# Kernel tuning notes

Measured on AMD Instinct MI355X. Metric: run time of the kernel, lower is better.

## Reference

```python
import jax, jax.numpy as jnp
import numpy as np
from jax import lax

NUM_CLASSES = 21      # VOC: background (class 0) + 20 fg classes
TOP_K = 200           # max detections kept per (image, class)
CONF_THRESH = 0.01
NMS_THRESH = 0.45
VAR0, VAR1 = 0.1, 0.2 # cfg.VARIANCE
K_PRE = 256           # candidates pre-selected per class before NMS (fixed-shape NMS)


def setup_inputs() -> dict:
    key = jax.random.key(0)
    k1, k2, k3 = jax.random.split(key, 3)
    B, P, C = 32, 8732, NUM_CLASSES
    loc_data = jax.random.normal(k1, (B, P, 4), dtype=jnp.float32)
    conf_data = jax.random.normal(k2, (B, P, C), dtype=jnp.float32)
    u = jax.random.uniform(k3, (P, 4), dtype=jnp.float32)
    # priors in center-offset form: centers in [0,1), w/h in [0.02, 0.32)
    prior_data = jnp.concatenate([u[:, :2], 0.02 + 0.3 * u[:, 2:]], axis=-1)
    return {"loc_data": loc_data, "conf_data": conf_data, "prior_data": prior_data}


def decode(loc, priors):
    # loc, priors: [..., 4]; priors are (cx, cy, w, h)
    centers = priors[..., :2] + loc[..., :2] * VAR0 * priors[..., 2:]
    wh = priors[..., 2:] * jnp.exp(loc[..., 2:] * VAR1)
    xy_min = centers - wh * 0.5
    return jnp.concatenate([xy_min, xy_min + wh], axis=-1)  # (x1,y1,x2,y2)


def pairwise_iou(b):
    # b: [K, 4] corner boxes -> [K, K] IoU
    area = jnp.maximum(b[:, 2] - b[:, 0], 0.0) * jnp.maximum(b[:, 3] - b[:, 1], 0.0)
    lt = jnp.maximum(b[:, None, :2], b[None, :, :2])
    rb = jnp.minimum(b[:, None, 2:], b[None, :, 2:])
    wh = jnp.clip(rb - lt, 0.0)
    inter = wh[..., 0] * wh[..., 1]
    union = area[:, None] + area[None, :] - inter
    return inter / jnp.maximum(union, 1e-9)


def nms_one_class(scores_p, boxes_p4):
    # scores_p: [P], boxes_p4: [P, 4]; fixed-shape NMS -> [TOP_K, 5] (score, x1, y1, x2, y2)
    vals, idx = lax.top_k(scores_p, K_PRE)          # sorted descending
    cand = boxes_p4[idx]                            # [K_PRE, 4]
    valid = vals > CONF_THRESH
    iou = pairwise_iou(cand)                        # [K_PRE, K_PRE]
    ar = jnp.arange(K_PRE)

    def step(keep, i):
        # a kept box suppresses later boxes overlapping it above threshold
        sup = keep[i] & (iou[i] > NMS_THRESH) & (ar > i)
        return keep & (~sup), None

    keep, _ = lax.scan(step, valid, ar)
    kept_scores = jnp.where(keep, vals, 0.0)
    # kept entries are already score-ordered; pull the top TOP_K survivors to the front
    sv, si = lax.top_k(kept_scores, TOP_K)
    out_boxes = jnp.where(sv[:, None] > 0.0, cand[si], 0.0)
    return jnp.concatenate([sv[:, None], out_boxes], axis=-1)  # [TOP_K, 5]


def reference(loc_data, conf_data, prior_data):
    # loc_data: [B, P, 4], conf_data: [B, P, C], prior_data: [P, 4]
    probs = jax.nn.softmax(conf_data, axis=-1)                     # [B, P, C]
    probs_fg = jnp.swapaxes(probs[..., 1:], 1, 2)                  # [B, C-1, P] (skip background)
    boxes = decode(loc_data, prior_data[None, :, :])               # [B, P, 4]
    # vmap over classes, then over batch
    per_class = jax.vmap(nms_one_class, in_axes=(0, None))         # ([C-1,P],[P,4]) -> [C-1,TOP_K,5]
    per_image = jax.vmap(per_class, in_axes=(0, 0))
    return per_image(probs_fg, boxes)                              # [B, C-1, TOP_K, 5]
```

## Files before the change

kernel.cpp:

```cpp
#include <hip/hip_runtime.h>
#include <stdint.h>

typedef unsigned long long ull;

#define NUM_CLASSES 21
#define NFG 20
#define TOPK 200
#define KPRE 256
#define CONF_TH 0.01f
#define NMS_TH 0.45f
#define VAR0 0.1f
#define VAR1 0.2f
#define NVMAX 35
#define BITS_CONF 0x3C23D70Au
#define BITS_ONE1 0x3F800001u
#define BSLOT(g) ((g) + ((g) >> 6))

__global__ __launch_bounds__(256) void softmax_probs_kernel(
    const float* __restrict__ conf, float* __restrict__ probs, int P) {
    __shared__ __align__(16) float obuf[NFG * 256];
    const int t = threadIdx.x;
    const int b = blockIdx.y;
    const int p0 = blockIdx.x << 8;
    const int cnt = min(256, P - p0);

    if (t < cnt) {
        const float* row = conf + ((size_t)b * P + p0 + t) * NUM_CLASSES;
        float x[NUM_CLASSES];
        float mx = row[0];
        x[0] = mx;
#pragma unroll
        for (int j = 1; j < NUM_CLASSES; ++j) { x[j] = row[j]; mx = fmaxf(mx, x[j]); }
        float s = 0.f;
#pragma unroll
        for (int j = 0; j < NUM_CLASSES; ++j) { x[j] = expf(x[j] - mx); s += x[j]; }
#pragma unroll
        for (int c = 1; c < NUM_CLASSES; ++c)
            obuf[(c - 1) * 256 + t] = x[c] / s;
    }
    __syncthreads();

    float* dst = probs + ((size_t)b * NFG) * P + p0;
    if (cnt == 256) {
#pragma unroll
        for (int k = 0; k < 5; ++k) {
            int e = (k << 8) + t;
            int c = e >> 6;
            int f = e & 63;
            float4 val = ((const float4*)obuf)[(c << 6) + f];
            *(float4*)(dst + (size_t)c * P + (f << 2)) = val;
        }
    } else {
        for (int e = t; e < NFG * cnt; e += 256) {
            int c = e / cnt;
            int f = e - c * cnt;
            dst[(size_t)c * P + f] = obuf[c * 256 + f];
        }
    }
}

__global__ __launch_bounds__(KPRE) void nms_topk_kernel(
    const float* __restrict__ probs, const float* __restrict__ loc,
    const float* __restrict__ prior, float* __restrict__ out, int B, int P) {

    __shared__ ull arr[2 * KPRE];
    __shared__ ull arr2[2 * KPRE];
    __shared__ int wsum[2][4];
    __shared__ int s_cnt;
    __shared__ float4 sbox[KPRE + (KPRE >> 6)];
    __shared__ float sarea[KPRE + (KPRE >> 6)];
    __shared__ ull smask[KPRE][5];
    __shared__ ull kept_mask[4];

    const int t = threadIdx.x;
    const int lane = t & 63;
    const int wid = t >> 6;
    const ull lmask_lt = (1ULL << lane) - 1ULL;

    const int g = blockIdx.x;
    int b, c;
    if ((B & 7) == 0) {
        int k = g >> 3;
        b = ((k / NFG) << 3) + (g & 7);
        c = k - (k / NFG) * NFG;
    } else {
        b = g / NFG;
        c = g - (g / NFG) * NFG;
    }
    const int pair = b * NFG + c;
    const float* sp = probs + (size_t)pair * P;

    unsigned int ubits[NVMAX];
#pragma unroll
    for (int i = 0; i < NVMAX; ++i) {
        int p = (i << 8) + t;
        ubits[i] = (p < P) ? __float_as_uint(sp[p]) : 0u;
    }

    {
        unsigned int lo = BITS_CONF, hi = BITS_ONE1;
        while (hi - lo > 1u) {
            unsigned int mid = lo + ((hi - lo) >> 1);
            int cc = 0;
#pragma unroll
            for (int i = 0; i < NVMAX; ++i)
                cc += __popcll(__ballot(ubits[i] >= mid));
            if (cc >= KPRE / 4) lo = mid; else hi = mid;
        }
        if (lane == 0) wsum[0][wid] = (int)lo;
    }
    __syncthreads();
    unsigned int T = (unsigned int)min(min(wsum[0][0], wsum[0][1]),
                                       min(wsum[0][2], wsum[0][3]));

    int nval;
    for (int attempt = 0;; ++attempt) {
        if (t == 0) s_cnt = 0;
        __syncthreads();
        int wtot = 0;
#pragma unroll
        for (int i = 0; i < NVMAX; ++i) {
            int p = (i << 8) + t;
            bool pred = (p < P) && (ubits[i] >= T);
            wtot += __popcll(__ballot(pred));
        }
        int wbase = 0;
        if (lane == 0) wbase = atomicAdd(&s_cnt, wtot);
        wbase = __shfl(wbase, 0);
        int run = wbase;
#pragma unroll
        for (int i = 0; i < NVMAX; ++i) {
            int p = (i << 8) + t;
            bool pred = (p < P) && (ubits[i] >= T);
            ull bal = __ballot(pred);
            if (pred) {
                int slot = run + __popcll(bal & lmask_lt);
                if (slot < 2 * KPRE)
                    arr[slot] = ((ull)ubits[i] << 32) | (unsigned int)(~p);
            }
            run += __popcll(bal);
        }
        __syncthreads();
        if (s_cnt <= 2 * KPRE || attempt == 1) { nval = min(s_cnt, 2 * KPRE); break; }
        unsigned int lo = T, hi = BITS_ONE1;
        int it = 0;
        while (hi - lo > 1u) {
            unsigned int mid = lo + ((hi - lo) >> 1);
            int cc = 0;
#pragma unroll
            for (int i = 0; i < NVMAX; ++i)
                cc += __popcll(__ballot(ubits[i] >= mid));
            if (lane == 0) wsum[it & 1][wid] = cc;
            __syncthreads();
            int totc = wsum[it & 1][0] + wsum[it & 1][1] + wsum[it & 1][2] + wsum[it & 1][3];
            if (totc >= KPRE) lo = mid; else hi = mid;
            ++it;
        }
        T = lo;
    }

    for (int e = t; e < 2 * KPRE; e += KPRE)
        if (e >= nval) arr[e] = 0ULL;
    __syncthreads();

    ull k0 = arr[t];
    ull k1 = arr[t + KPRE];
    {
        int lstage = 0;
#pragma unroll
        for (int kk = 2; kk <= 2 * KPRE; kk <<= 1) {
#pragma unroll
            for (int j = kk >> 1; j > 0; j >>= 1) {
                if (j == KPRE) {
                    ull mx = (k0 > k1) ? k0 : k1;
                    ull mn = (k0 > k1) ? k1 : k0;
                    k0 = mx; k1 = mn;
                } else if (j >= 64) {
                    ull* A = (lstage & 1) ? arr : arr2;
                    ++lstage;
                    A[t] = k0; A[t + KPRE] = k1;
                    __syncthreads();
                    ull o0 = A[t ^ j];
                    ull o1 = A[(t + KPRE) ^ j];
                    bool amLow = ((t & j) == 0);
                    bool d0 = ((t & kk) == 0);
                    bool d1 = (((t + KPRE) & kk) == 0);
                    k0 = (d0 == amLow) ? ((k0 > o0) ? k0 : o0) : ((k0 > o0) ? o0 : k0);
                    k1 = (d1 == amLow) ? ((k1 > o1) ? k1 : o1) : ((k1 > o1) ? o1 : k1);
                } else {
                    ull o0 = __shfl_xor(k0, j);
                    ull o1 = __shfl_xor(k1, j);
                    bool amLow = ((t & j) == 0);
                    bool d0 = ((t & kk) == 0);
                    bool d1 = (((t + KPRE) & kk) == 0);
                    k0 = (d0 == amLow) ? ((k0 > o0) ? k0 : o0) : ((k0 > o0) ? o0 : k0);
                    k1 = (d1 == amLow) ? ((k1 > o1) ? k1 : o1) : ((k1 > o1) ? o1 : k1);
                }
            }
        }
    }
    const ull key = k0;

    float v = __uint_as_float((unsigned int)(key >> 32));
    int idx = (int)(~(unsigned int)(key & 0xFFFFFFFFu));
    if (idx < 0 || idx >= P) { idx = 0; v = 0.f; }

    const float4 lv = *(const float4*)(loc + ((size_t)b * P + idx) * 4);
    const float4 pv = *(const float4*)(prior + (size_t)idx * 4);
    float cx = pv.x + (lv.x * VAR0) * pv.z;
    float cy = pv.y + (lv.y * VAR0) * pv.w;
    float w = pv.z * expf(lv.z * VAR1);
    float h = pv.w * expf(lv.w * VAR1);
    float x1 = cx - w * 0.5f;
    float y1 = cy - h * 0.5f;
    float x2 = x1 + w;
    float y2 = y1 + h;
    float myarea = fmaxf(x2 - x1, 0.f) * fmaxf(y2 - y1, 0.f);

    sbox[BSLOT(t)] = make_float4(x1, y1, x2, y2);
    sarea[BSLOT(t)] = myarea;
    __syncthreads();

#pragma unroll
    for (int rep = 0; rep < 3; ++rep) {
        int pid = t + (rep << 8);
        if (pid < 640) {
            int r, w2;
            if (pid < 64)       { r = pid;                w2 = 0; }
            else if (pid < 192) { int q = pid - 64;  r = 64  + (q >> 1); w2 = q & 1; }
            else if (pid < 384) { int q = pid - 192; int q3 = q / 3; r = 128 + q3; w2 = q - 3 * q3; }
            else                { int q = pid - 384; r = 192 + (q >> 2); w2 = q & 3; }
            float4 rb = sbox[BSLOT(r)];
            float ra = sarea[BSLOT(r)];
            ull mm = 0ULL;
            for (int i = 0; i < 64; ++i) {
                int gg = (w2 << 6) + i;
                float4 gb = sbox[BSLOT(gg)];
                float lx = fmaxf(gb.x, rb.x), ly = fmaxf(gb.y, rb.y);
                float rx = fminf(gb.z, rb.z), ry = fminf(gb.w, rb.w);
                float iw = fmaxf(rx - lx, 0.f), ih = fmaxf(ry - ly, 0.f);
                float inter = iw * ih;
                float uni = sarea[BSLOT(gg)] + ra - inter;
                bool s = (inter / fmaxf(uni, 1e-9f)) > NMS_TH;
                mm |= ((ull)(s ? 1u : 0u)) << i;
            }
            smask[r][w2] = mm;
        }
    }
    __syncthreads();

    ull m0 = smask[t][0];
    ull m1 = (wid >= 1) ? smask[t][1] : 0ULL;
    ull m2 = (wid >= 2) ? smask[t][2] : 0ULL;
    ull m3 = (wid >= 3) ? smask[t][3] : 0ULL;
    if (wid == 0) m0 &= lmask_lt;
    else if (wid == 1) m1 &= lmask_lt;
    else if (wid == 2) m2 &= lmask_lt;
    else m3 &= lmask_lt;

    int alive = (v > CONF_TH) ? 1 : 0;
    ull mykept = 0ULL;
#pragma unroll
    for (int w2 = 0; w2 < 4; ++w2) {
        if (wid == w2) {
            if (w2 > 0 && (m0 & kept_mask[0])) alive = 0;
            if (w2 > 1 && (m1 & kept_mask[1])) alive = 0;
            if (w2 > 2 && (m2 & kept_mask[2])) alive = 0;
            ull mw = (w2 == 0) ? m0 : (w2 == 1) ? m1 : (w2 == 2) ? m2 : m3;
            ull validb = __ballot(alive != 0);
            ull todo = __ballot((mw & validb) != 0ULL) & validb;
            ull kept = validb & ~todo;
            while (todo) {
                int i = __builtin_ctzll(todo);
                ull row = __shfl(mw, i);
                if ((row & kept) == 0ULL) kept |= (1ULL << i);
                todo &= (todo - 1ULL);
            }
            mykept = kept;
            alive = (int)((kept >> lane) & 1ULL);
            if (lane == 0) kept_mask[w2] = kept;
        }
        __syncthreads();
    }

    int rank = 0;
#pragma unroll
    for (int w2 = 0; w2 < 4; ++w2)
        if (w2 < wid) rank += __popcll(kept_mask[w2]);
    rank += __popcll(mykept & lmask_lt);
    int total = 0;
#pragma unroll
    for (int w2 = 0; w2 < 4; ++w2) total += __popcll(kept_mask[w2]);

    float* orow = out + (size_t)pair * TOPK * 5;
    if (alive && rank < TOPK) {
        float* o = orow + rank * 5;
        o[0] = v; o[1] = x1; o[2] = y1; o[3] = x2; o[4] = y2;
    }
    if (t < TOPK && t >= total) {
        float* o = orow + t * 5;
        o[0] = 0.f; o[1] = 0.f; o[2] = 0.f; o[3] = 0.f; o[4] = 0.f;
    }
}

extern "C" void kernel_launch(void* const* d_in, const int* in_sizes, int n_in,
                              void* d_out, int out_size, void* d_ws, size_t ws_size,
                              hipStream_t stream) {
    const float* loc = (const float*)d_in[0];
    const float* conf = (const float*)d_in[1];
    const float* prior = (const float*)d_in[2];
    float* out = (float*)d_out;
    float* probs = (float*)d_ws;

    int P = in_sizes[2] / 4;
    int B = in_sizes[0] / (4 * P);

    dim3 g1((P + 255) / 256, B);
    softmax_probs_kernel<<<g1, 256, 0, stream>>>(conf, probs, P);
    nms_topk_kernel<<<B * NFG, KPRE, 0, stream>>>(probs, loc, prior, out, B, P);
}
```

Baseline: 135.3 us.

## Fuse softmax into NMS kernel with a grid-wide atomic barrier

Merges the softmax pass into the NMS kernel. Each of the B*NFG blocks computes softmax for a slice of priors of its image, then all blocks wait at a software grid barrier built on a global atomic counter before the per-class NMS reads the probabilities. This removes one kernel launch and the gap between the two kernels. In exchange the softmax writes are now uncoalesced strided stores rather than going through a shared-memory transpose, and the barrier only works if all 640 blocks are resident at the same time, otherwise it deadlocks.

Result: slower. 299.1 us (+121.1%).

```diff
diff --git a/kernel.cpp b/kernel.cpp
--- a/kernel.cpp
+++ b/kernel.cpp
@@ -16,52 +16,12 @@
 #define BITS_ONE1 0x3F800001u
 #define BSLOT(g) ((g) + ((g) >> 6))
 
-__global__ __launch_bounds__(256) void softmax_probs_kernel(
-    const float* __restrict__ conf, float* __restrict__ probs, int P) {
-    __shared__ __align__(16) float obuf[NFG * 256];
-    const int t = threadIdx.x;
-    const int b = blockIdx.y;
-    const int p0 = blockIdx.x << 8;
-    const int cnt = min(256, P - p0);
-
-    if (t < cnt) {
-        const float* row = conf + ((size_t)b * P + p0 + t) * NUM_CLASSES;
-        float x[NUM_CLASSES];
-        float mx = row[0];
-        x[0] = mx;
-#pragma unroll
-        for (int j = 1; j < NUM_CLASSES; ++j) { x[j] = row[j]; mx = fmaxf(mx, x[j]); }
-        float s = 0.f;
-#pragma unroll
-        for (int j = 0; j < NUM_CLASSES; ++j) { x[j] = expf(x[j] - mx); s += x[j]; }
-#pragma unroll
-        for (int c = 1; c < NUM_CLASSES; ++c)
-            obuf[(c - 1) * 256 + t] = x[c] / s;
-    }
-    __syncthreads();
-
-    float* dst = probs + ((size_t)b * NFG) * P + p0;
-    if (cnt == 256) {
-#pragma unroll
-        for (int k = 0; k < 5; ++k) {
-            int e = (k << 8) + t;
-            int c = e >> 6;
-            int f = e & 63;
-            float4 val = ((const float4*)obuf)[(c << 6) + f];
-            *(float4*)(dst + (size_t)c * P + (f << 2)) = val;
-        }
-    } else {
-        for (int e = t; e < NFG * cnt; e += 256) {
-            int c = e / cnt;
-            int f = e - c * cnt;
-            dst[(size_t)c * P + f] = obuf[c * 256 + f];
-        }
-    }
-}
-
-__global__ __launch_bounds__(KPRE) void nms_topk_kernel(
-    const float* __restrict__ probs, const float* __restrict__ loc,
-    const float* __restrict__ prior, float* __restrict__ out, int B, int P) {
+__device__ unsigned int g_bar = 0u;
+
+__global__ __launch_bounds__(KPRE) void fused_postproc_kernel(
+    const float* __restrict__ conf, const float* __restrict__ loc,
+    const float* __restrict__ prior, float* __restrict__ probs,
+    float* __restrict__ out, int B, int P) {
 
     __shared__ ull arr[2 * KPRE];
     __shared__ ull arr2[2 * KPRE];
@@ -88,6 +48,43 @@
         c = g - (g / NFG) * NFG;
     }
     const int pair = b * NFG + c;
+
+    {
+        const int RPB = (P + NFG - 1) / NFG;
+        const int r0 = c * RPB;
+        const int rend = min(r0 + RPB, P);
+        for (int p = r0 + t; p < rend; p += KPRE) {
+            const float* row = conf + ((size_t)b * P + p) * NUM_CLASSES;
+            float x[NUM_CLASSES];
+            float mx = row[0];
+            x[0] = mx;
+#pragma unroll
+            for (int j = 1; j < NUM_CLASSES; ++j) { x[j] = row[j]; mx = fmaxf(mx, x[j]); }
+            float s = 0.f;
+#pragma unroll
+            for (int j = 0; j < NUM_CLASSES; ++j) { x[j] = expf(x[j] - mx); s += x[j]; }
+            float* dp = probs + ((size_t)b * NFG) * P + p;
+#pragma unroll
+            for (int c2 = 1; c2 < NUM_CLASSES; ++c2)
+                dp[(size_t)(c2 - 1) * P] = x[c2] / s;
+        }
+    }
+
+    {
+        const unsigned int nblk = gridDim.x;
+        __threadfence();
+        __syncthreads();
+        if (t == 0) {
+            unsigned int old = atomicAdd(&g_bar, 1u);
+            unsigned int target = (old / nblk + 1u) * nblk;
+            while (__hip_atomic_load(&g_bar, __ATOMIC_RELAXED,
+                                     __HIP_MEMORY_SCOPE_AGENT) < target)
+                __builtin_amdgcn_s_sleep(8);
+        }
+        __syncthreads();
+        __threadfence();
+    }
+
     const float* sp = probs + (size_t)pair * P;
 
     unsigned int ubits[NVMAX];
@@ -315,7 +312,6 @@
     int P = in_sizes[2] / 4;
     int B = in_sizes[0] / (4 * P);
 
-    dim3 g1((P + 255) / 256, B);
-    softmax_probs_kernel<<<g1, 256, 0, stream>>>(conf, probs, P);
-    nms_topk_kernel<<<B * NFG, KPRE, 0, stream>>>(probs, loc, prior, out, B, P);
+    fused_postproc_kernel<<<dim3(B * NFG), dim3(KPRE), 0, stream>>>(
+        conf, loc, prior, probs, out, B, P);
 }
```

## Stage softmax input through LDS and vectorize probability loads in NMS

Applied to the files above, without the earlier changes.

The softmax kernel now copies each block's contiguous slab of confidence logits into shared memory with coalesced non-temporal float4 loads. Each thread then reads its row from LDS, instead of doing per-thread strided row loads from global memory. The NMS kernel loads per-class probabilities as float4 vectors and remaps each register slot to its prior index, so that element indices and tie-breaking stay the same. The aim is to cut memory transaction overhead on both input paths. The vector path assumes P is a multiple of four and that buffers are 16-byte aligned, and it adds an extra LDS pass and barrier in the softmax kernel.

Measured after the change: 139.9 us. 3.5% more time.

```diff
diff --git a/kernel.cpp b/kernel.cpp
--- a/kernel.cpp
+++ b/kernel.cpp
@@ -2,6 +2,7 @@
 #include <stdint.h>
 
 typedef unsigned long long ull;
+typedef float f4v __attribute__((ext_vector_type(4)));
 
 #define NUM_CLASSES 21
 #define NFG 20
@@ -11,21 +12,39 @@
 #define NMS_TH 0.45f
 #define VAR0 0.1f
 #define VAR1 0.2f
-#define NVMAX 35
+#define NV4 9
+#define NVAL 36
 #define BITS_CONF 0x3C23D70Au
 #define BITS_ONE1 0x3F800001u
 #define BSLOT(g) ((g) + ((g) >> 6))
 
 __global__ __launch_bounds__(256) void softmax_probs_kernel(
     const float* __restrict__ conf, float* __restrict__ probs, int P) {
-    __shared__ __align__(16) float obuf[NFG * 256];
+    __shared__ __align__(16) float buf[256 * NUM_CLASSES];
     const int t = threadIdx.x;
     const int b = blockIdx.y;
     const int p0 = blockIdx.x << 8;
     const int cnt = min(256, P - p0);
-
+    const float* src = conf + ((size_t)b * P + p0) * NUM_CLASSES;
+
+    if (cnt == 256) {
+        const f4v* s4 = (const f4v*)src;
+        f4v* b4 = (f4v*)buf;
+#pragma unroll
+        for (int k = 0; k < 6; ++k) {
+            int i = (k << 8) + t;
+            if (i < (256 * NUM_CLASSES) / 4)
+                b4[i] = __builtin_nontemporal_load(s4 + i);
+        }
+    } else {
+        int n = cnt * NUM_CLASSES;
+        for (int i = t; i < n; i += 256) buf[i] = src[i];
+    }
+    __syncthreads();
+
+    float sc[NFG];
     if (t < cnt) {
-        const float* row = conf + ((size_t)b * P + p0 + t) * NUM_CLASSES;
+        const float* row = buf + t * NUM_CLASSES;
         float x[NUM_CLASSES];
         float mx = row[0];
         x[0] = mx;
@@ -36,7 +55,14 @@
         for (int j = 0; j < NUM_CLASSES; ++j) { x[j] = expf(x[j] - mx); s += x[j]; }
 #pragma unroll
         for (int c = 1; c < NUM_CLASSES; ++c)
-            obuf[(c - 1) * 256 + t] = x[c] / s;
+            sc[c - 1] = x[c] / s;
+    }
+    __syncthreads();
+
+    if (t < cnt) {
+#pragma unroll
+        for (int c = 0; c < NFG; ++c)
+            buf[c * 256 + t] = sc[c];
     }
     __syncthreads();
 
@@ -47,14 +73,14 @@
             int e = (k << 8) + t;
             int c = e >> 6;
             int f = e & 63;
-            float4 val = ((const float4*)obuf)[(c << 6) + f];
+            float4 val = ((const float4*)buf)[(c << 6) + f];
             *(float4*)(dst + (size_t)c * P + (f << 2)) = val;
         }
     } else {
         for (int e = t; e < NFG * cnt; e += 256) {
             int c = e / cnt;
             int f = e - c * cnt;
-            dst[(size_t)c * P + f] = obuf[c * 256 + f];
+            dst[(size_t)c * P + f] = buf[c * 256 + f];
         }
     }
 }
@@ -89,13 +115,26 @@
     }
     const int pair = b * NFG + c;
     const float* sp = probs + (size_t)pair * P;
-
-    unsigned int ubits[NVMAX];
-#pragma unroll
-    for (int i = 0; i < NVMAX; ++i) {
-        int p = (i << 8) + t;
-        ubits[i] = (p < P) ? __float_as_uint(sp[p]) : 0u;
-    }
+    const int nq4 = P >> 2;
+
+    unsigned int ubits[NVAL];
+    {
+        const f4v* sp4 = (const f4v*)sp;
+#pragma unroll
+        for (int j = 0; j < NV4; ++j) {
+            int q = (j << 8) + t;
+            if (q < nq4) {
+                f4v v = sp4[q];
+#pragma unroll
+                for (int e = 0; e < 4; ++e)
+                    ubits[j * 4 + e] = __float_as_uint(v[e]);
+            } else {
+#pragma unroll
+                for (int e = 0; e < 4; ++e) ubits[j * 4 + e] = 0u;
+            }
+        }
+    }
+#define PIDX(i) ((((i) >> 2) << 10) + (t << 2) + ((i) & 3))
 
     {
         unsigned int lo = BITS_CONF, hi = BITS_ONE1;
@@ -103,7 +142,7 @@
             unsigned int mid = lo + ((hi - lo) >> 1);
             int cc = 0;
 #pragma unroll
-            for (int i = 0; i < NVMAX; ++i)
+            for (int i = 0; i < NVAL; ++i)
                 cc += __popcll(__ballot(ubits[i] >= mid));
             if (cc >= KPRE / 4) lo = mid; else hi = mid;
         }
@@ -119,8 +158,8 @@
         __syncthreads();
         int wtot = 0;
 #pragma unroll
-        for (int i = 0; i < NVMAX; ++i) {
-            int p = (i << 8) + t;
+        for (int i = 0; i < NVAL; ++i) {
+            int p = PIDX(i);
             bool pred = (p < P) && (ubits[i] >= T);
             wtot += __popcll(__ballot(pred));
         }
@@ -129,8 +168,8 @@
         wbase = __shfl(wbase, 0);
         int run = wbase;
 #pragma unroll
-        for (int i = 0; i < NVMAX; ++i) {
-            int p = (i << 8) + t;
+        for (int i = 0; i < NVAL; ++i) {
+            int p = PIDX(i);
             bool pred = (p < P) && (ubits[i] >= T);
             ull bal = __ballot(pred);
             if (pred) {
@@ -148,7 +187,7 @@
             unsigned int mid = lo + ((hi - lo) >> 1);
             int cc = 0;
 #pragma unroll
-            for (int i = 0; i < NVMAX; ++i)
+            for (int i = 0; i < NVAL; ++i)
                 cc += __popcll(__ballot(ubits[i] >= mid));
             if (lane == 0) wsum[it & 1][wid] = cc;
             __syncthreads();
@@ -301,6 +340,7 @@
         float* o = orow + t * 5;
         o[0] = 0.f; o[1] = 0.f; o[2] = 0.f; o[3] = 0.f; o[4] = 0.f;
     }
+#undef PIDX
 }
 
 extern "C" void kernel_launch(void* const* d_in, const int* in_sizes, int n_in,
```

## Stage softmax input through LDS with coalesced nontemporal loads, coarsen threshold search

Applied to the files above, without the earlier changes.

The softmax kernel now loads each 256-row chunk of conf into shared memory with coalesced 16-byte nontemporal loads instead of strided per-thread row reads. It writes probabilities with nontemporal stores and remaps the 1D grid so that batches interleave in groups of 8. The per-wave threshold binary search in the NMS kernel now works on the top 16 bits of the float, which cuts the number of ballot iterations. The coarser threshold is lower, so more candidates may pass and trigger the refinement pass more often, and the larger LDS buffer may reduce occupancy.

After: 130.4 us. 1.04x faster.

```diff
diff --git a/kernel.cpp b/kernel.cpp
--- a/kernel.cpp
+++ b/kernel.cpp
@@ -2,6 +2,7 @@
 #include <stdint.h>
 
 typedef unsigned long long ull;
+typedef float f4v __attribute__((ext_vector_type(4)));
 
 #define NUM_CLASSES 21
 #define NFG 20
@@ -13,19 +14,47 @@
 #define VAR1 0.2f
 #define NVMAX 35
 #define BITS_CONF 0x3C23D70Au
-#define BITS_ONE1 0x3F800001u
 #define BSLOT(g) ((g) + ((g) >> 6))
 
 __global__ __launch_bounds__(256) void softmax_probs_kernel(
-    const float* __restrict__ conf, float* __restrict__ probs, int P) {
-    __shared__ __align__(16) float obuf[NFG * 256];
+    const float* __restrict__ conf, float* __restrict__ probs, int B, int P) {
+    __shared__ __align__(16) float buf[256 * NUM_CLASSES];
     const int t = threadIdx.x;
-    const int b = blockIdx.y;
-    const int p0 = blockIdx.x << 8;
+    const int nch = (P + 255) >> 8;
+
+    const int id = blockIdx.x;
+    int b, chk;
+    if ((B & 7) == 0) {
+        int r = id & 7, m = id >> 3;
+        int q = m / nch;
+        b = r + (q << 3);
+        chk = m - q * nch;
+    } else {
+        b = id / nch;
+        chk = id - b * nch;
+    }
+    const int p0 = chk << 8;
     const int cnt = min(256, P - p0);
-
+    const float* src = conf + ((size_t)b * P + p0) * NUM_CLASSES;
+
+    if (cnt == 256) {
+        const f4v* s4 = (const f4v*)src;
+        f4v* b4 = (f4v*)buf;
+#pragma unroll
+        for (int k = 0; k < 6; ++k) {
+            int i = (k << 8) + t;
+            if (i < (256 * NUM_CLASSES) / 4)
+                b4[i] = __builtin_nontemporal_load(s4 + i);
+        }
+    } else {
+        int n = cnt * NUM_CLASSES;
+        for (int i = t; i < n; i += 256) buf[i] = src[i];
+    }
+    __syncthreads();
+
+    float sc[NFG];
     if (t < cnt) {
-        const float* row = conf + ((size_t)b * P + p0 + t) * NUM_CLASSES;
+        const float* row = buf + t * NUM_CLASSES;
         float x[NUM_CLASSES];
         float mx = row[0];
         x[0] = mx;
@@ -36,7 +65,14 @@
         for (int j = 0; j < NUM_CLASSES; ++j) { x[j] = expf(x[j] - mx); s += x[j]; }
 #pragma unroll
         for (int c = 1; c < NUM_CLASSES; ++c)
-            obuf[(c - 1) * 256 + t] = x[c] / s;
+            sc[c - 1] = x[c] / s;
+    }
+    __syncthreads();
+
+    if (t < cnt) {
+#pragma unroll
+        for (int c = 0; c < NFG; ++c)
+            buf[c * 256 + t] = sc[c];
     }
     __syncthreads();
 
@@ -47,14 +83,14 @@
             int e = (k << 8) + t;
             int c = e >> 6;
             int f = e & 63;
-            float4 val = ((const float4*)obuf)[(c << 6) + f];
-            *(float4*)(dst + (size_t)c * P + (f << 2)) = val;
+            f4v val = ((const f4v*)buf)[(c << 6) + f];
+            __builtin_nontemporal_store(val, (f4v*)(dst + (size_t)c * P + (f << 2)));
         }
     } else {
         for (int e = t; e < NFG * cnt; e += 256) {
             int c = e / cnt;
             int f = e - c * cnt;
-            dst[(size_t)c * P + f] = obuf[c * 256 + f];
+            __builtin_nontemporal_store(buf[c * 256 + f], dst + (size_t)c * P + f);
         }
     }
 }
@@ -98,16 +134,17 @@
     }
 
     {
-        unsigned int lo = BITS_CONF, hi = BITS_ONE1;
+        unsigned int lo = 0x3C23u, hi = 0x3F81u;
         while (hi - lo > 1u) {
             unsigned int mid = lo + ((hi - lo) >> 1);
+            unsigned int m32 = mid << 16;
             int cc = 0;
 #pragma unroll
             for (int i = 0; i < NVMAX; ++i)
-                cc += __popcll(__ballot(ubits[i] >= mid));
+                cc += __popcll(__ballot(ubits[i] >= m32));
             if (cc >= KPRE / 4) lo = mid; else hi = mid;
         }
-        if (lane == 0) wsum[0][wid] = (int)lo;
+        if (lane == 0) wsum[0][wid] = (int)(lo << 16);
     }
     __syncthreads();
     unsigned int T = (unsigned int)min(min(wsum[0][0], wsum[0][1]),
@@ -142,7 +179,7 @@
         }
         __syncthreads();
         if (s_cnt <= 2 * KPRE || attempt == 1) { nval = min(s_cnt, 2 * KPRE); break; }
-        unsigned int lo = T, hi = BITS_ONE1;
+        unsigned int lo = T, hi = 0x3F800001u;
         int it = 0;
         while (hi - lo > 1u) {
             unsigned int mid = lo + ((hi - lo) >> 1);
@@ -314,8 +351,8 @@
 
     int P = in_sizes[2] / 4;
     int B = in_sizes[0] / (4 * P);
-
-    dim3 g1((P + 255) / 256, B);
-    softmax_probs_kernel<<<g1, 256, 0, stream>>>(conf, probs, P);
+    int nch = (P + 255) / 256;
+
+    softmax_probs_kernel<<<dim3(B * nch), 256, 0, stream>>>(conf, probs, B, P);
     nms_topk_kernel<<<B * NFG, KPRE, 0, stream>>>(probs, loc, prior, out, B, P);
 }
```
